# Optimization experiments

Measured on AMD Instinct MI355X. Metric: run time of the kernel, lower is better.

## Reference

```python
import jax, jax.numpy as jnp
import numpy as np
from jax import lax

D_MODEL = 256
VOCAB = 512
D_INNER = 512          # expand=2
D_STATE = 64
D_CONV = 4
HEADDIM = 32
NHEADS = D_INNER // HEADDIM  # 16
NGROUPS = 1
CHUNK = 64
D_IN_PROJ = 2 * D_INNER + 2 * NGROUPS * D_STATE + NHEADS  # 1168
CONV_DIM = D_INNER + 2 * NGROUPS * D_STATE               # 640


def setup_inputs() -> dict:
    key = jax.random.key(0)
    ks = jax.random.split(key, 8)
    B, L = 8, 4096
    input_ids = jax.random.randint(ks[0], (B, L), 0, VOCAB)
    rn = lambda k, shp, sc: (jax.random.normal(k, shp) * sc).astype(jnp.float32)
    embed_w = rn(ks[1], (VOCAB, D_MODEL), 0.02).at[0].set(0.0)  # padding_idx=0
    in_proj_w = rn(ks[2], (D_IN_PROJ, D_MODEL), D_MODEL ** -0.5)
    conv_w = rn(ks[3], (CONV_DIM, D_CONV), 0.2)
    conv_b = jnp.zeros((CONV_DIM,), jnp.float32)
    A_log = jnp.log(jax.random.uniform(ks[4], (NHEADS,), minval=1.0, maxval=16.0)).astype(jnp.float32)
    D_skip = jnp.ones((NHEADS,), jnp.float32)
    dt0 = jax.random.uniform(ks[5], (NHEADS,), minval=1e-3, maxval=0.1)
    dt_bias = jnp.log(jnp.expm1(dt0)).astype(jnp.float32)  # inverse softplus
    gate_norm_w = jnp.ones((D_INNER,), jnp.float32)
    out_proj_w = rn(ks[6], (D_MODEL, D_INNER), D_INNER ** -0.5)
    norm_w = jnp.ones((D_MODEL,), jnp.float32)
    return dict(input_ids=input_ids, embed_w=embed_w, in_proj_w=in_proj_w,
                conv_w=conv_w, conv_b=conv_b, A_log=A_log, D_skip=D_skip,
                dt_bias=dt_bias, gate_norm_w=gate_norm_w, out_proj_w=out_proj_w,
                norm_w=norm_w)


def _rmsnorm(x, w, eps):
    return x * lax.rsqrt(jnp.mean(x * x, axis=-1, keepdims=True) + eps) * w


def _segsum(a):
    # a: (..., T) -> (..., T, T); out[q,s] = sum_{s+1..q} a, -inf above diag
    T = a.shape[-1]
    c = jnp.cumsum(a, axis=-1)
    seg = c[..., :, None] - c[..., None, :]
    mask = jnp.tril(jnp.ones((T, T), bool))
    return jnp.where(mask, seg, -jnp.inf)


def _ssd(X, A, Bm, Cm):
    # X:(b,l,h,p) already *dt ; A:(b,l,h)=dt*A_head ; Bm,Cm:(b,l,n)
    b, l, h, p = X.shape
    n = Bm.shape[-1]
    c, q = l // CHUNK, CHUNK
    X = X.reshape(b, c, q, h, p)
    A = A.reshape(b, c, q, h).transpose(0, 3, 1, 2)        # (b,h,c,q)
    Bm = Bm.reshape(b, c, q, n)
    Cm = Cm.reshape(b, c, q, n)
    A_cs = jnp.cumsum(A, axis=-1)                           # (b,h,c,q)
    Lmat = jnp.exp(_segsum(A))                              # (b,h,c,q,q)
    # intra-chunk (diagonal block) output
    Y_diag = jnp.einsum('bcqn,bckn,bhcqk,bckhp->bcqhp', Cm, Bm, Lmat, X)
    # states carried to end of each chunk
    decay_states = jnp.exp(A_cs[..., -1:] - A_cs)           # (b,h,c,q)
    states = jnp.einsum('bckn,bhck,bckhp->bchpn', Bm, decay_states, X)
    chunk_decay = jnp.exp(A_cs[..., -1])                    # (b,h,c)
    def step(hprev, inp):
        dec, st = inp
        return dec[..., None, None] * hprev + st, hprev
    _, prev = lax.scan(step, jnp.zeros((b, h, p, n), X.dtype),
                       (chunk_decay.transpose(2, 0, 1), states.transpose(1, 0, 2, 3, 4)))
    prev = prev.transpose(1, 0, 2, 3, 4)                    # (b,c,h,p,n)
    Y_off = jnp.einsum('bcqn,bchpn,bhcq->bcqhp', Cm, prev, jnp.exp(A_cs))
    return (Y_diag + Y_off).reshape(b, l, h, p)


def _mamba2(u, in_proj_w, conv_w, conv_b, A_log, D_skip, dt_bias, gate_norm_w, out_proj_w):
    B, L, _ = u.shape
    zxbcdt = u @ in_proj_w.T                                # (B,L,1168)
    z = zxbcdt[..., :D_INNER]
    xBC = zxbcdt[..., D_INNER:D_INNER + CONV_DIM]
    dt = zxbcdt[..., D_INNER + CONV_DIM:]                   # (B,L,H)
    # causal depthwise conv + silu
    xBC = lax.conv_general_dilated(xBC.transpose(0, 2, 1), conv_w[:, None, :],
                                   (1,), [(D_CONV - 1, 0)],
                                   dimension_numbers=('NCH', 'OIH', 'NCH'),
                                   feature_group_count=CONV_DIM)
    xBC = jax.nn.silu(xBC + conv_b[None, :, None]).transpose(0, 2, 1)
    x = xBC[..., :D_INNER].reshape(B, L, NHEADS, HEADDIM)
    Bm = xBC[..., D_INNER:D_INNER + D_STATE]
    Cm = xBC[..., D_INNER + D_STATE:]
    dt = jax.nn.softplus(dt + dt_bias)                      # (B,L,H)
    A = -jnp.exp(A_log)                                     # (H,)
    y = _ssd(x * dt[..., None], dt * A, Bm, Cm)
    y = y + D_skip[None, None, :, None] * x
    y = y.reshape(B, L, D_INNER)
    y = _rmsnorm(y * jax.nn.silu(z), gate_norm_w, 1e-5)     # RMSNormGated
    return y @ out_proj_w.T


def reference(input_ids, embed_w, in_proj_w, conv_w, conv_b, A_log, D_skip,
              dt_bias, gate_norm_w, out_proj_w, norm_w):
    x = embed_w[input_ids]                                  # (B,L,D)
    u = _rmsnorm(x, norm_w, 1e-6)
    x = x + _mamba2(u, in_proj_w, conv_w, conv_b, A_log, D_skip,
                    dt_bias, gate_norm_w, out_proj_w)
    logits = x @ embed_w.T                                  # tied lm_head
    return logits
```

## Files before the change

### kernel.cpp

```cpp
#include <hip/hip_runtime.h>
#include <cstdint>
#include <cstddef>

#define TOK    32768
#define BATCH  8
#define SEQ    4096
#define DMODEL 256
#define DINNER 512
#define DSTATE 64
#define NH     16
#define HD     32
#define DPROJ  1168
#define NPAD   1280
#define CONVD  640
#define VOCAB  512
#define HGRP   4
#define TS     132

typedef __attribute__((ext_vector_type(8))) short bf16x8;
typedef __attribute__((ext_vector_type(4))) float f32x4;

__device__ __forceinline__ unsigned short f2bf(float f) {
    unsigned u = __float_as_uint(f);
    u += 0x7fffu + ((u >> 16) & 1u);
    return (unsigned short)(u >> 16);
}
__device__ __forceinline__ float bf2f(short s) {
    return __uint_as_float(((unsigned)(unsigned short)s) << 16);
}
__device__ __forceinline__ unsigned cvtpk(float lo, float hi) {
    unsigned r;
    asm("v_cvt_pk_bf16_f32 %0, %1, %2" : "=v"(r) : "v"(lo), "v"(hi));
    return r;
}
__device__ __forceinline__ float fsilu(float s) {
    return s * __builtin_amdgcn_rcpf(1.f + __expf(-s));
}
__device__ __forceinline__ float sp(float v) {
    return v > 20.f ? v : __logf(1.f + __expf(v));
}

__device__ __forceinline__ void gload16(const short* src, short* dst) {
    __builtin_amdgcn_global_load_lds((const __attribute__((address_space(1))) void*)src,
                                     (__attribute__((address_space(3))) void*)dst, 16, 0, 0);
}

#define U16_OFF   0
#define Z16_OFF   (U16_OFF  + (size_t)TOK*128)
#define XBC_OFF   (Z16_OFF  + (size_t)TOK*256)
#define DTS_OFF   (XBC_OFF  + (size_t)TOK*320)
#define ACS_OFF   (DTS_OFF  + (size_t)TOK*16)
#define CDEC_OFF  (ACS_OFF  + (size_t)BATCH*NH*64*64)
#define WP_OFF    (CDEC_OFF + (size_t)BATCH*NH*64)
#define WO_OFF    (WP_OFF   + 163840)
#define WE_OFF    (WO_OFF   + 65536)
#define UNION_OFF (WE_OFF   + 65536)
#define UNION_FL  ((size_t)BATCH*64*NH*2048)
#define XF_SUB    ((size_t)TOK*256)
#define WS_FLOATS (UNION_OFF + UNION_FL)

__global__ void k_diag(float* out, float wsmb) {
    if (blockIdx.x == 0 && threadIdx.x == 0) out[0] = wsmb;
}

__global__ void k_cvt(const float* __restrict__ s, short* __restrict__ d, int nsrc, int ntot) {
    int i = blockIdx.x * 256 + threadIdx.x;
    if (i < ntot) d[i] = (i < nsrc) ? (short)f2bf(s[i]) : (short)0;
}

__global__ void k_embed(const int* __restrict__ ids, const float* __restrict__ embed,
                        const float* __restrict__ norm_w, short* __restrict__ u16) {
    int t = blockIdx.x;
    int lane = threadIdx.x;
    int id = ids[t];
    float4 v = ((const float4*)(embed + (size_t)id * DMODEL))[lane];
    float ss = v.x*v.x + v.y*v.y + v.z*v.z + v.w*v.w;
    #pragma unroll
    for (int o = 32; o > 0; o >>= 1) ss += __shfl_down(ss, o);
    ss = __shfl(ss, 0);
    float r = rsqrtf(ss * (1.0f / DMODEL) + 1e-6f);
    float4 w = ((const float4*)norm_w)[lane];
    unsigned p0 = cvtpk(v.x * r * w.x, v.y * r * w.y);
    unsigned p1 = cvtpk(v.z * r * w.z, v.w * r * w.w);
    ((uint2*)(u16 + (size_t)t * DMODEL))[lane] = make_uint2(p0, p1);
}

template<int MODE>
__global__ __launch_bounds__(512) void k_gemm_mfma(
    const short* __restrict__ A, const short* __restrict__ B, int K,
    float* __restrict__ outF, short* __restrict__ z16, short* __restrict__ xbc,
    float* __restrict__ dts, const float* __restrict__ dt_bias,
    const int* __restrict__ ids, const float* __restrict__ embed,
    const float* __restrict__ cw, const float* __restrict__ cb) {
    __shared__ __align__(16) short SM[32768];
    int tid = threadIdx.x;
    int m0 = blockIdx.y << 7;
    int n0 = blockIdx.x << 7;
    int wave = tid >> 6, lane = tid & 63;
    int wm = wave >> 1, wn = wave & 1;
    int lr = lane & 15, lg = lane >> 4;
    const f32x4 zer = {0.f, 0.f, 0.f, 0.f};
    f32x4 acc[2][4];
    #pragma unroll
    for (int i = 0; i < 2; i++)
        #pragma unroll
        for (int j = 0; j < 4; j++) acc[i][j] = zer;

    const bool isXBC = (MODE == 0) && (n0 >= 512) && (n0 < 1152);
    const bool atStart = (m0 & (SEQ - 1)) == 0;
    const bool haloLane = isXBC && (wm == 0) && !atStart && (lr < 3);
    f32x4 hacc[4];
    #pragma unroll
    for (int j = 0; j < 4; j++) hacc[j] = zer;
    const bf16x8 hz = {0, 0, 0, 0, 0, 0, 0, 0};
    bf16x8 hc0 = hz, hc1 = hz, hn0 = hz, hn1 = hz;

    const int nK = K >> 6;
    const int slo = lane >> 3;
    const int skb = ((lane & 7) ^ slo) << 3;

    {
        #pragma unroll
        for (int j = 0; j < 2; j++) {
            int row = wave * 16 + j * 8 + slo;
            gload16(A + (size_t)(m0 + row) * K + skb, SM + (wave * 2 + j) * 512);
            gload16(B + (size_t)(n0 + row) * K + skb, SM + 16384 + (wave * 2 + j) * 512);
        }
        if (haloLane) {
            hc0 = *(const bf16x8*)(A + (size_t)(m0 - 3 + lr) * K + lg * 8);
            hc1 = *(const bf16x8*)(A + (size_t)(m0 - 3 + lr) * K + 32 + lg * 8);
        }
    }
    __syncthreads();

    for (int kt = 0; kt < nK; ++kt) {
        if (kt + 1 < nK) {
            int k0 = (kt + 1) << 6;
            int nb = ((kt + 1) & 1) * 8192;
            #pragma unroll
            for (int j = 0; j < 2; j++) {
                int row = wave * 16 + j * 8 + slo;
                gload16(A + (size_t)(m0 + row) * K + k0 + skb, SM + nb + (wave * 2 + j) * 512);
                gload16(B + (size_t)(n0 + row) * K + k0 + skb, SM + 16384 + nb + (wave * 2 + j) * 512);
            }
            if (haloLane) {
                hn0 = *(const bf16x8*)(A + (size_t)(m0 - 3 + lr) * K + k0 + lg * 8);
                hn1 = *(const bf16x8*)(A + (size_t)(m0 - 3 + lr) * K + k0 + 32 + lg * 8);
            }
        }
        const short* CA = SM + (kt & 1) * 8192;
        const short* CB = SM + 16384 + (kt & 1) * 8192;
        #pragma unroll
        for (int kk = 0; kk < 2; kk++) {
            int sw = (((kk << 2) + lg) ^ (lr & 7)) << 3;
            bf16x8 af[2], bfr[4];
            #pragma unroll
            for (int mi = 0; mi < 2; mi++)
                af[mi] = *(const bf16x8*)&CA[(wm * 32 + mi * 16 + lr) * 64 + sw];
            #pragma unroll
            for (int ni = 0; ni < 4; ni++)
                bfr[ni] = *(const bf16x8*)&CB[(wn * 64 + ni * 16 + lr) * 64 + sw];
            #pragma unroll
            for (int mi = 0; mi < 2; mi++)
                #pragma unroll
                for (int ni = 0; ni < 4; ni++)
                    acc[mi][ni] = __builtin_amdgcn_mfma_f32_16x16x32_bf16(af[mi], bfr[ni], acc[mi][ni], 0, 0, 0);
            if (isXBC && wm == 0) {
                bf16x8 h = (kk == 0) ? hc0 : hc1;
                #pragma unroll
                for (int ni = 0; ni < 4; ni++)
                    hacc[ni] = __builtin_amdgcn_mfma_f32_16x16x32_bf16(h, bfr[ni], hacc[ni], 0, 0, 0);
            }
        }
        __syncthreads();
        hc0 = hn0; hc1 = hn1;
    }

    if (isXBC) {
        short* Tile = SM;
        #pragma unroll
        for (int mi = 0; mi < 2; mi++)
            #pragma unroll
            for (int ni = 0; ni < 4; ni++)
                #pragma unroll
                for (int r = 0; r < 4; r++) {
                    int row = wm * 32 + mi * 16 + lg * 4 + r;
                    int col = wn * 64 + ni * 16 + lr;
                    float v = acc[mi][ni][r];
                    float vo = __shfl_xor(v, 1);
                    if (!(lr & 1))
                        *(unsigned*)&Tile[(3 + row) * TS + col] = cvtpk(v, vo);
                }
        if (wm == 0 && lg == 0) {
            #pragma unroll
            for (int ni = 0; ni < 4; ni++)
                #pragma unroll
                for (int r = 0; r < 3; r++)
                    Tile[r * TS + wn * 64 + ni * 16 + lr] = (short)f2bf(hacc[ni][r]);
        }
        __syncthreads();
        int cp = tid & 63, rg = tid >> 6;
        int colb = cp * 2;
        int ch = (n0 - 512) + colb;
        float c0w0 = cw[ch * 4], c0w1 = cw[ch * 4 + 1], c0w2 = cw[ch * 4 + 2], c0w3 = cw[ch * 4 + 3];
        float c1w0 = cw[ch * 4 + 4], c1w1 = cw[ch * 4 + 5], c1w2 = cw[ch * 4 + 6], c1w3 = cw[ch * 4 + 7];
        float b0v = cb[ch], b1v = cb[ch + 1];
        int rbase = rg * 16;
        unsigned w0 = *(const unsigned*)&Tile[(rbase + 0) * TS + colb];
        unsigned w1 = *(const unsigned*)&Tile[(rbase + 1) * TS + colb];
        unsigned w2 = *(const unsigned*)&Tile[(rbase + 2) * TS + colb];
        for (int i = 0; i < 16; i++) {
            unsigned w3 = *(const unsigned*)&Tile[(rbase + i + 3) * TS + colb];
            float s0 = b0v, s1 = b1v;
            s0 = fmaf(bf2f((short)(w0 & 0xffffu)), c0w0, s0); s1 = fmaf(bf2f((short)(w0 >> 16)), c1w0, s1);
            s0 = fmaf(bf2f((short)(w1 & 0xffffu)), c0w1, s0); s1 = fmaf(bf2f((short)(w1 >> 16)), c1w1, s1);
            s0 = fmaf(bf2f((short)(w2 & 0xffffu)), c0w2, s0); s1 = fmaf(bf2f((short)(w2 >> 16)), c1w2, s1);
            s0 = fmaf(bf2f((short)(w3 & 0xffffu)), c0w3, s0); s1 = fmaf(bf2f((short)(w3 >> 16)), c1w3, s1);
            s0 = fsilu(s0);
            s1 = fsilu(s1);
            *(unsigned*)&xbc[(size_t)(m0 + rbase + i) * CONVD + ch] = cvtpk(s0, s1);
            w0 = w1; w1 = w2; w2 = w3;
        }
        return;
    }

    #pragma unroll
    for (int mi = 0; mi < 2; mi++) {
        #pragma unroll
        for (int r = 0; r < 4; r++) {
            int row = m0 + wm * 32 + mi * 16 + lg * 4 + r;
            int id = 0;
            if (MODE == 1) id = ids[row];
            #pragma unroll
            for (int ni = 0; ni < 4; ni++) {
                int col = n0 + wn * 64 + ni * 16 + lr;
                float v = acc[mi][ni][r];
                if (MODE == 0) {
                    if (n0 < 512) {
                        float vo = __shfl_xor(v, 1);
                        if (!(lr & 1))
                            *(unsigned*)&z16[(size_t)row * DINNER + col] = cvtpk(v, vo);
                    } else if (wn == 0 && ni == 0) {
                        dts[(size_t)row * NH + lr] = sp(v + dt_bias[lr]);
                    }
                } else if (MODE == 1) {
                    float vo = __shfl_xor(v, 1);
                    if (!(lr & 1)) {
                        float2 res = *(const float2*)&embed[(size_t)id * DMODEL + col];
                        *(unsigned*)&z16[(size_t)row * DMODEL + col] = cvtpk(v + res.x, vo + res.y);
                    }
                } else {
                    outF[(size_t)row * VOCAB + col] = v;
                }
            }
        }
    }
}

__global__ __launch_bounds__(256) void k_states(const short* __restrict__ xbc, const float* __restrict__ dts,
                                                const float* __restrict__ A_log,
                                                short* __restrict__ st16,
                                                float* __restrict__ acs_g, float* __restrict__ cdec) {
    __shared__ short BsB[64 * 72];
    __shared__ short BT[64 * 72];
    __shared__ short XdS[32 * 72];
    __shared__ float dkS[HGRP][64];
    int tid = threadIdx.x;
    int bid = blockIdx.x;
    int hg = bid & 3;
    int bc = bid >> 2;
    int b = bc >> 6, c = bc & 63;
    int h0 = hg * HGRP;
    size_t tbase = (size_t)b * SEQ + (size_t)c * 64;
    int wave = tid >> 6, lane = tid & 63;
    int lr = lane & 15, lg = lane >> 4;

    for (int i = tid; i < 64 * 64; i += 256) {
        int q = i >> 6, n = i & 63;
        BsB[q * 72 + n] = xbc[(tbase + q) * CONVD + DINNER + n];
    }
    {
        int h = h0 + wave;
        float Ah = -__expf(A_log[h]);
        float v = dts[(tbase + lane) * NH + h] * Ah;
        #pragma unroll
        for (int off = 1; off < 64; off <<= 1) {
            float o = __shfl_up(v, off);
            if (lane >= off) v += o;
        }
        acs_g[(((size_t)(b * NH + h)) * 64 + c) * 64 + lane] = v;
        float alast = __shfl(v, 63);
        dkS[wave][lane] = __expf(alast - v);
        if (lane == 0) cdec[(b * NH + h) * 64 + c] = __expf(alast);
    }
    __syncthreads();
    for (int i = tid; i < 64 * 64; i += 256) {
        int k = i >> 6, n = i & 63;
        BT[n * 72 + k] = BsB[k * 72 + n];
    }
    __syncthreads();

    for (int hh = 0; hh < HGRP; hh++) {
        int h = h0 + hh;
        for (int i = tid; i < 2048; i += 256) {
            int p = i & 31, k = i >> 5;
            float xv = bf2f(xbc[(tbase + k) * CONVD + h * HD + p]);
            XdS[p * 72 + k] = (short)f2bf(xv * dts[(tbase + k) * NH + h] * dkS[hh][k]);
        }
        __syncthreads();
        {
            int ptile = wave & 1;
            bf16x8 a0 = *(const bf16x8*)&XdS[(ptile * 16 + lr) * 72 + lg * 8];
            bf16x8 a1 = *(const bf16x8*)&XdS[(ptile * 16 + lr) * 72 + 32 + lg * 8];
            size_t base = ((size_t)bc * NH + h) * 2048;
            #pragma unroll
            for (int j = 0; j < 2; j++) {
                int nt = (wave >> 1) * 2 + j;
                bf16x8 b0 = *(const bf16x8*)&BT[(nt * 16 + lr) * 72 + lg * 8];
                bf16x8 b1 = *(const bf16x8*)&BT[(nt * 16 + lr) * 72 + 32 + lg * 8];
                f32x4 z = {0.f, 0.f, 0.f, 0.f};
                z = __builtin_amdgcn_mfma_f32_16x16x32_bf16(a0, b0, z, 0, 0, 0);
                z = __builtin_amdgcn_mfma_f32_16x16x32_bf16(a1, b1, z, 0, 0, 0);
                #pragma unroll
                for (int r = 0; r < 4; r++) {
                    int p = ptile * 16 + lg * 4 + r;
                    float v = z[r];
                    float vo = __shfl_xor(v, 1);
                    if (!(lr & 1))
                        *(unsigned*)&st16[base + p * 64 + nt * 16 + lr] = cvtpk(v, vo);
                }
            }
        }
        __syncthreads();
    }
}

__global__ __launch_bounds__(256) void k_scan(unsigned* __restrict__ st32, const float* __restrict__ cdec) {
    int bid = blockIdx.x;
    int bh = bid >> 2, seg = bid & 3;
    int b = bh >> 4, h = bh & 15;
    int off = seg * 256 + threadIdx.x;
    float p0 = 0.f, p1 = 0.f;
    for (int c = 0; c < 64; c++) {
        float dec = cdec[bh * 64 + c];
        size_t idx = ((((size_t)b * 64 + c) * NH) + h) * 1024 + off;
        unsigned v = st32[idx];
        float s0 = bf2f((short)(v & 0xffffu));
        float s1 = bf2f((short)(v >> 16));
        st32[idx] = cvtpk(p0, p1);
        p0 = fmaf(dec, p0, s0);
        p1 = fmaf(dec, p1, s1);
    }
}

__global__ __launch_bounds__(256) void k_y(const short* __restrict__ xbc, const float* __restrict__ dts,
                                           const short* __restrict__ st16, const float* __restrict__ acs_g,
                                           const float* __restrict__ D_skip, float* __restrict__ Y) {
    __shared__ short CsB[64 * 72];
    __shared__ short BsB[64 * 72];
    __shared__ short Wsh[64 * 72];
    __shared__ short XtS[32 * 72];
    __shared__ short Pt[32 * 72];
    __shared__ float acsS[HGRP][64];
    int tid = threadIdx.x;
    int bid = blockIdx.x;
    int hg = bid & 3;
    int bc = bid >> 2;
    int b = bc >> 6, c = bc & 63;
    int h0 = hg * HGRP;
    size_t tbase = (size_t)b * SEQ + (size_t)c * 64;
    int wave = tid >> 6, lane = tid & 63;
    int lr = lane & 15, lg = lane >> 4;

    for (int i = tid; i < 64 * 64; i += 256) {
        int q = i >> 6, n = i & 63;
        const short* rowp = xbc + (tbase + q) * CONVD + DINNER;
        BsB[q * 72 + n] = rowp[n];
        CsB[q * 72 + n] = rowp[DSTATE + n];
    }
    acsS[wave][lane] = acs_g[(((size_t)(b * NH + h0 + wave)) * 64 + c) * 64 + lane];
    __syncthreads();

    f32x4 macc[4];
    {
        bf16x8 aw0 = *(const bf16x8*)&CsB[(wave * 16 + lr) * 72 + lg * 8];
        bf16x8 aw1 = *(const bf16x8*)&CsB[(wave * 16 + lr) * 72 + 32 + lg * 8];
        #pragma unroll
        for (int ct = 0; ct < 4; ct++) {
            bf16x8 b0 = *(const bf16x8*)&BsB[(ct * 16 + lr) * 72 + lg * 8];
            bf16x8 b1 = *(const bf16x8*)&BsB[(ct * 16 + lr) * 72 + 32 + lg * 8];
            f32x4 z = {0.f, 0.f, 0.f, 0.f};
            z = __builtin_amdgcn_mfma_f32_16x16x32_bf16(aw0, b0, z, 0, 0, 0);
            z = __builtin_amdgcn_mfma_f32_16x16x32_bf16(aw1, b1, z, 0, 0, 0);
            macc[ct] = z;
        }
    }

    for (int hh = 0; hh < HGRP; hh++) {
        int h = h0 + hh;
        #pragma unroll
        for (int ct = 0; ct < 4; ct++) {
            int k = ct * 16 + lr;
            #pragma unroll
            for (int r = 0; r < 4; r++) {
                int q = wave * 16 + lg * 4 + r;
                float wv = 0.f;
                if (k <= q) wv = macc[ct][r] * __expf(acsS[hh][q] - acsS[hh][k]);
                float wo = __shfl_xor(wv, 1);
                if (!(lr & 1))
                    *(unsigned*)&Wsh[q * 72 + k] = cvtpk(wv, wo);
            }
        }
        for (int i = tid; i < 2048; i += 256) {
            int p = i & 31, k = i >> 5;
            float xv = bf2f(xbc[(tbase + k) * CONVD + h * HD + p]);
            XtS[p * 72 + k] = (short)f2bf(xv * dts[(tbase + k) * NH + h]);
        }
        size_t sbase = ((size_t)bc * NH + h) * 2048;
        for (int i = tid; i < 2048; i += 256)
            Pt[(i >> 6) * 72 + (i & 63)] = st16[sbase + i];
        __syncthreads();
        float eq[4];
        #pragma unroll
        for (int r = 0; r < 4; r++) eq[r] = __expf(acsS[hh][wave * 16 + lg * 4 + r]);
        float dsk = D_skip[h];
        bf16x8 wa0 = *(const bf16x8*)&Wsh[(wave * 16 + lr) * 72 + lg * 8];
        bf16x8 wa1 = *(const bf16x8*)&Wsh[(wave * 16 + lr) * 72 + 32 + lg * 8];
        bf16x8 ca0 = *(const bf16x8*)&CsB[(wave * 16 + lr) * 72 + lg * 8];
        bf16x8 ca1 = *(const bf16x8*)&CsB[(wave * 16 + lr) * 72 + 32 + lg * 8];
        #pragma unroll
        for (int pt = 0; pt < 2; pt++) {
            bf16x8 xb0 = *(const bf16x8*)&XtS[(pt * 16 + lr) * 72 + lg * 8];
            bf16x8 xb1 = *(const bf16x8*)&XtS[(pt * 16 + lr) * 72 + 32 + lg * 8];
            f32x4 zd = {0.f, 0.f, 0.f, 0.f};
            zd = __builtin_amdgcn_mfma_f32_16x16x32_bf16(wa0, xb0, zd, 0, 0, 0);
            zd = __builtin_amdgcn_mfma_f32_16x16x32_bf16(wa1, xb1, zd, 0, 0, 0);
            bf16x8 pb0 = *(const bf16x8*)&Pt[(pt * 16 + lr) * 72 + lg * 8];
            bf16x8 pb1 = *(const bf16x8*)&Pt[(pt * 16 + lr) * 72 + 32 + lg * 8];
            f32x4 zo = {0.f, 0.f, 0.f, 0.f};
            zo = __builtin_amdgcn_mfma_f32_16x16x32_bf16(ca0, pb0, zo, 0, 0, 0);
            zo = __builtin_amdgcn_mfma_f32_16x16x32_bf16(ca1, pb1, zo, 0, 0, 0);
            #pragma unroll
            for (int r = 0; r < 4; r++) {
                int q = wave * 16 + lg * 4 + r;
                int p = pt * 16 + lr;
                float xv = bf2f(xbc[(tbase + q) * CONVD + h * HD + p]);
                Y[((tbase + q) * NH + h) * HD + p] = zd[r] + eq[r] * zo[r] + dsk * xv;
            }
        }
        __syncthreads();
    }
}

__global__ void k_gate(const float* __restrict__ Y, const short* __restrict__ z16,
                       const float* __restrict__ gw, short* __restrict__ Yb) {
    int t = blockIdx.x;
    int lane = threadIdx.x;
    const float* yr = Y + (size_t)t * DINNER + lane * 8;
    union { int4 v; short s[8]; } zu;
    zu.v = *(const int4*)(z16 + (size_t)t * DINNER + lane * 8);
    float4 y0 = *(const float4*)yr;
    float4 y1 = *(const float4*)(yr + 4);
    float yv[8] = {y0.x, y0.y, y0.z, y0.w, y1.x, y1.y, y1.z, y1.w};
    float g[8];
    float ss = 0.f;
    #pragma unroll
    for (int i = 0; i < 8; i++) {
        float zf = bf2f(zu.s[i]);
        g[i] = yv[i] * fsilu(zf);
        ss += g[i] * g[i];
    }
    #pragma unroll
    for (int o = 32; o > 0; o >>= 1) ss += __shfl_down(ss, o);
    ss = __shfl(ss, 0);
    float rr = rsqrtf(ss * (1.0f / DINNER) + 1e-5f);
    const float* wr = gw + lane * 8;
    float4 w0 = *(const float4*)wr;
    float4 w1 = *(const float4*)(wr + 4);
    float wv[8] = {w0.x, w0.y, w0.z, w0.w, w1.x, w1.y, w1.z, w1.w};
    union { uint4 v; unsigned u[4]; } ou;
    #pragma unroll
    for (int i = 0; i < 4; i++)
        ou.u[i] = cvtpk(g[2*i] * rr * wv[2*i], g[2*i+1] * rr * wv[2*i+1]);
    *(uint4*)(Yb + (size_t)t * DINNER + lane * 8) = ou.v;
}

extern "C" void kernel_launch(void* const* d_in, const int* in_sizes, int n_in,
                              void* d_out, int out_size, void* d_ws, size_t ws_size,
                              hipStream_t stream) {
    const int*   ids        = (const int*)d_in[0];
    const float* embed_w    = (const float*)d_in[1];
    const float* in_proj_w  = (const float*)d_in[2];
    const float* conv_w     = (const float*)d_in[3];
    const float* conv_b     = (const float*)d_in[4];
    const float* A_log      = (const float*)d_in[5];
    const float* D_skip     = (const float*)d_in[6];
    const float* dt_bias    = (const float*)d_in[7];
    const float* gate_w     = (const float*)d_in[8];
    const float* out_proj_w = (const float*)d_in[9];
    const float* norm_w     = (const float*)d_in[10];
    float* out = (float*)d_out;

    if (ws_size < WS_FLOATS * sizeof(float)) {
        k_diag<<<1, 64, 0, stream>>>(out, (float)(ws_size >> 20));
        return;
    }

    float* ws   = (float*)d_ws;
    short* u16  = (short*)(ws + U16_OFF);
    short* z16  = (short*)(ws + Z16_OFF);
    short* xbc  = (short*)(ws + XBC_OFF);
    float* dts  = ws + DTS_OFF;
    float* acs  = ws + ACS_OFF;
    float* cdec = ws + CDEC_OFF;
    short* Wp   = (short*)(ws + WP_OFF);
    short* Wo   = (short*)(ws + WO_OFF);
    short* We   = (short*)(ws + WE_OFF);
    short* st16 = (short*)(ws + UNION_OFF);
    short* Yb   = (short*)(ws + UNION_OFF);
    short* xf16 = (short*)(ws + UNION_OFF + XF_SUB);
    float* Y    = out;

    k_cvt<<<(NPAD * DMODEL + 255) / 256, 256, 0, stream>>>(in_proj_w, Wp, DPROJ * DMODEL, NPAD * DMODEL);
    k_cvt<<<(DMODEL * DINNER + 255) / 256, 256, 0, stream>>>(out_proj_w, Wo, DMODEL * DINNER, DMODEL * DINNER);
    k_cvt<<<(VOCAB * DMODEL + 255) / 256, 256, 0, stream>>>(embed_w, We, VOCAB * DMODEL, VOCAB * DMODEL);
    k_embed<<<TOK, 64, 0, stream>>>(ids, embed_w, norm_w, u16);
    k_gemm_mfma<0><<<dim3(NPAD / 128, TOK / 128), 512, 0, stream>>>(
        u16, Wp, DMODEL, nullptr, z16, xbc, dts, dt_bias, nullptr, nullptr, conv_w, conv_b);
    k_states<<<BATCH * 64 * 4, 256, 0, stream>>>(xbc, dts, A_log, st16, acs, cdec);
    k_scan<<<BATCH * NH * 4, 256, 0, stream>>>((unsigned*)st16, cdec);
    k_y<<<BATCH * 64 * 4, 256, 0, stream>>>(xbc, dts, st16, acs, D_skip, Y);
    k_gate<<<TOK, 64, 0, stream>>>(Y, z16, gate_w, Yb);
    k_gemm_mfma<1><<<dim3(DMODEL / 128, TOK / 128), 512, 0, stream>>>(
        Yb, Wo, DINNER, nullptr, xf16, nullptr, nullptr, nullptr, ids, embed_w, nullptr, nullptr);
    k_gemm_mfma<2><<<dim3(VOCAB / 128, TOK / 128), 512, 0, stream>>>(
        xf16, We, DMODEL, out, nullptr, nullptr, nullptr, nullptr, nullptr, nullptr, nullptr, nullptr);
}
```

Baseline: 255.5 us.

## Store SSD output as bf16 and process heads in pairs to halve barriers

k_y now writes its per-head output as packed bf16 into workspace instead of fp32 into the output buffer, and k_gate reads bf16, which halves the intermediate Y traffic. Both k_states and k_y now stage two heads per iteration with double LDS buffers, halving the number of __syncthreads rounds and giving more independent MFMA work between barriers. k_y also hoists the C-operand fragments out of the head loop. The cost is extra LDS per block, which may lower occupancy, and an added bf16 rounding of Y before the gated RMSNorm.

```diff
diff --git a/kernel.cpp b/kernel.cpp
--- a/kernel.cpp
+++ b/kernel.cpp
@@ -56,6 +56,7 @@
 #define WE_OFF    (WO_OFF   + 65536)
 #define UNION_OFF (WE_OFF   + 65536)
 #define UNION_FL  ((size_t)BATCH*64*NH*2048)
+#define Y16_SUB   ((size_t)TOK*256)
 #define XF_SUB    ((size_t)TOK*256)
 #define WS_FLOATS (UNION_OFF + UNION_FL)
 
@@ -263,7 +264,8 @@
                                                 float* __restrict__ acs_g, float* __restrict__ cdec) {
     __shared__ short BsB[64 * 72];
     __shared__ short BT[64 * 72];
-    __shared__ short XdS[32 * 72];
+    __shared__ short Xd0[32 * 72];
+    __shared__ short Xd1[32 * 72];
     __shared__ float dkS[HGRP][64];
     int tid = threadIdx.x;
     int bid = blockIdx.x;
@@ -300,37 +302,44 @@
     }
     __syncthreads();
 
-    for (int hh = 0; hh < HGRP; hh++) {
-        int h = h0 + hh;
+    auto do_head = [&](int h, const short* Xd) {
+        int ptile = wave & 1;
+        bf16x8 a0 = *(const bf16x8*)&Xd[(ptile * 16 + lr) * 72 + lg * 8];
+        bf16x8 a1 = *(const bf16x8*)&Xd[(ptile * 16 + lr) * 72 + 32 + lg * 8];
+        size_t base = ((size_t)bc * NH + h) * 2048;
+        #pragma unroll
+        for (int j = 0; j < 2; j++) {
+            int nt = (wave >> 1) * 2 + j;
+            bf16x8 b0 = *(const bf16x8*)&BT[(nt * 16 + lr) * 72 + lg * 8];
+            bf16x8 b1 = *(const bf16x8*)&BT[(nt * 16 + lr) * 72 + 32 + lg * 8];
+            f32x4 z = {0.f, 0.f, 0.f, 0.f};
+            z = __builtin_amdgcn_mfma_f32_16x16x32_bf16(a0, b0, z, 0, 0, 0);
+            z = __builtin_amdgcn_mfma_f32_16x16x32_bf16(a1, b1, z, 0, 0, 0);
+            #pragma unroll
+            for (int r = 0; r < 4; r++) {
+                int p = ptile * 16 + lg * 4 + r;
+                float v = z[r];
+                float vo = __shfl_xor(v, 1);
+                if (!(lr & 1))
+                    *(unsigned*)&st16[base + p * 64 + nt * 16 + lr] = cvtpk(v, vo);
+            }
+        }
+    };
+
+    #pragma unroll
+    for (int pr = 0; pr < HGRP / 2; pr++) {
+        int hhA = pr * 2, hhB = hhA + 1;
+        int hA = h0 + hhA, hB = h0 + hhB;
         for (int i = tid; i < 2048; i += 256) {
             int p = i & 31, k = i >> 5;
-            float xv = bf2f(xbc[(tbase + k) * CONVD + h * HD + p]);
-            XdS[p * 72 + k] = (short)f2bf(xv * dts[(tbase + k) * NH + h] * dkS[hh][k]);
+            float dtA = dts[(tbase + k) * NH + hA];
+            float dtB = dts[(tbase + k) * NH + hB];
+            Xd0[p * 72 + k] = (short)f2bf(bf2f(xbc[(tbase + k) * CONVD + hA * HD + p]) * dtA * dkS[hhA][k]);
+            Xd1[p * 72 + k] = (short)f2bf(bf2f(xbc[(tbase + k) * CONVD + hB * HD + p]) * dtB * dkS[hhB][k]);
         }
         __syncthreads();
-        {
-            int ptile = wave & 1;
-            bf16x8 a0 = *(const bf16x8*)&XdS[(ptile * 16 + lr) * 72 + lg * 8];
-            bf16x8 a1 = *(const bf16x8*)&XdS[(ptile * 16 + lr) * 72 + 32 + lg * 8];
-            size_t base = ((size_t)bc * NH + h) * 2048;
-            #pragma unroll
-            for (int j = 0; j < 2; j++) {
-                int nt = (wave >> 1) * 2 + j;
-                bf16x8 b0 = *(const bf16x8*)&BT[(nt * 16 + lr) * 72 + lg * 8];
-                bf16x8 b1 = *(const bf16x8*)&BT[(nt * 16 + lr) * 72 + 32 + lg * 8];
-                f32x4 z = {0.f, 0.f, 0.f, 0.f};
-                z = __builtin_amdgcn_mfma_f32_16x16x32_bf16(a0, b0, z, 0, 0, 0);
-                z = __builtin_amdgcn_mfma_f32_16x16x32_bf16(a1, b1, z, 0, 0, 0);
-                #pragma unroll
-                for (int r = 0; r < 4; r++) {
-                    int p = ptile * 16 + lg * 4 + r;
-                    float v = z[r];
-                    float vo = __shfl_xor(v, 1);
-                    if (!(lr & 1))
-                        *(unsigned*)&st16[base + p * 64 + nt * 16 + lr] = cvtpk(v, vo);
-                }
-            }
-        }
+        do_head(hA, Xd0);
+        do_head(hB, Xd1);
         __syncthreads();
     }
 }
@@ -355,12 +364,12 @@
 
 __global__ __launch_bounds__(256) void k_y(const short* __restrict__ xbc, const float* __restrict__ dts,
                                            const short* __restrict__ st16, const float* __restrict__ acs_g,
-                                           const float* __restrict__ D_skip, float* __restrict__ Y) {
+                                           const float* __restrict__ D_skip, short* __restrict__ Y16) {
     __shared__ short CsB[64 * 72];
-    __shared__ short BsB[64 * 72];
-    __shared__ short Wsh[64 * 72];
-    __shared__ short XtS[32 * 72];
-    __shared__ short Pt[32 * 72];
+    __shared__ short W0[64 * 72];
+    __shared__ short W1[64 * 72];
+    __shared__ short Xt0[32 * 72], Xt1[32 * 72];
+    __shared__ short Pt0[32 * 72], Pt1[32 * 72];
     __shared__ float acsS[HGRP][64];
     int tid = threadIdx.x;
     int bid = blockIdx.x;
@@ -375,29 +384,29 @@
     for (int i = tid; i < 64 * 64; i += 256) {
         int q = i >> 6, n = i & 63;
         const short* rowp = xbc + (tbase + q) * CONVD + DINNER;
-        BsB[q * 72 + n] = rowp[n];
+        W0[q * 72 + n]  = rowp[n];
         CsB[q * 72 + n] = rowp[DSTATE + n];
     }
     acsS[wave][lane] = acs_g[(((size_t)(b * NH + h0 + wave)) * 64 + c) * 64 + lane];
     __syncthreads();
 
     f32x4 macc[4];
+    bf16x8 ca0 = *(const bf16x8*)&CsB[(wave * 16 + lr) * 72 + lg * 8];
+    bf16x8 ca1 = *(const bf16x8*)&CsB[(wave * 16 + lr) * 72 + 32 + lg * 8];
     {
-        bf16x8 aw0 = *(const bf16x8*)&CsB[(wave * 16 + lr) * 72 + lg * 8];
-        bf16x8 aw1 = *(const bf16x8*)&CsB[(wave * 16 + lr) * 72 + 32 + lg * 8];
         #pragma unroll
         for (int ct = 0; ct < 4; ct++) {
-            bf16x8 b0 = *(const bf16x8*)&BsB[(ct * 16 + lr) * 72 + lg * 8];
-            bf16x8 b1 = *(const bf16x8*)&BsB[(ct * 16 + lr) * 72 + 32 + lg * 8];
+            bf16x8 b0 = *(const bf16x8*)&W0[(ct * 16 + lr) * 72 + lg * 8];
+            bf16x8 b1 = *(const bf16x8*)&W0[(ct * 16 + lr) * 72 + 32 + lg * 8];
             f32x4 z = {0.f, 0.f, 0.f, 0.f};
-            z = __builtin_amdgcn_mfma_f32_16x16x32_bf16(aw0, b0, z, 0, 0, 0);
-            z = __builtin_amdgcn_mfma_f32_16x16x32_bf16(aw1, b1, z, 0, 0, 0);
+            z = __builtin_amdgcn_mfma_f32_16x16x32_bf16(ca0, b0, z, 0, 0, 0);
+            z = __builtin_amdgcn_mfma_f32_16x16x32_bf16(ca1, b1, z, 0, 0, 0);
             macc[ct] = z;
         }
     }
-
-    for (int hh = 0; hh < HGRP; hh++) {
-        int h = h0 + hh;
+    __syncthreads();
+
+    auto build_w = [&](int hh, short* Wb) {
         #pragma unroll
         for (int ct = 0; ct < 4; ct++) {
             int k = ct * 16 + lr;
@@ -408,30 +417,21 @@
                 if (k <= q) wv = macc[ct][r] * __expf(acsS[hh][q] - acsS[hh][k]);
                 float wo = __shfl_xor(wv, 1);
                 if (!(lr & 1))
-                    *(unsigned*)&Wsh[q * 72 + k] = cvtpk(wv, wo);
-            }
-        }
-        for (int i = tid; i < 2048; i += 256) {
-            int p = i & 31, k = i >> 5;
-            float xv = bf2f(xbc[(tbase + k) * CONVD + h * HD + p]);
-            XtS[p * 72 + k] = (short)f2bf(xv * dts[(tbase + k) * NH + h]);
-        }
-        size_t sbase = ((size_t)bc * NH + h) * 2048;
-        for (int i = tid; i < 2048; i += 256)
-            Pt[(i >> 6) * 72 + (i & 63)] = st16[sbase + i];
-        __syncthreads();
+                    *(unsigned*)&Wb[q * 72 + k] = cvtpk(wv, wo);
+            }
+        }
+    };
+    auto do_head = [&](int h, int hh, const short* Wb, const short* Xt, const short* Pt) {
         float eq[4];
         #pragma unroll
         for (int r = 0; r < 4; r++) eq[r] = __expf(acsS[hh][wave * 16 + lg * 4 + r]);
         float dsk = D_skip[h];
-        bf16x8 wa0 = *(const bf16x8*)&Wsh[(wave * 16 + lr) * 72 + lg * 8];
-        bf16x8 wa1 = *(const bf16x8*)&Wsh[(wave * 16 + lr) * 72 + 32 + lg * 8];
-        bf16x8 ca0 = *(const bf16x8*)&CsB[(wave * 16 + lr) * 72 + lg * 8];
-        bf16x8 ca1 = *(const bf16x8*)&CsB[(wave * 16 + lr) * 72 + 32 + lg * 8];
+        bf16x8 wa0 = *(const bf16x8*)&Wb[(wave * 16 + lr) * 72 + lg * 8];
+        bf16x8 wa1 = *(const bf16x8*)&Wb[(wave * 16 + lr) * 72 + 32 + lg * 8];
         #pragma unroll
         for (int pt = 0; pt < 2; pt++) {
-            bf16x8 xb0 = *(const bf16x8*)&XtS[(pt * 16 + lr) * 72 + lg * 8];
-            bf16x8 xb1 = *(const bf16x8*)&XtS[(pt * 16 + lr) * 72 + 32 + lg * 8];
+            bf16x8 xb0 = *(const bf16x8*)&Xt[(pt * 16 + lr) * 72 + lg * 8];
+            bf16x8 xb1 = *(const bf16x8*)&Xt[(pt * 16 + lr) * 72 + 32 + lg * 8];
             f32x4 zd = {0.f, 0.f, 0.f, 0.f};
             zd = __builtin_amdgcn_mfma_f32_16x16x32_bf16(wa0, xb0, zd, 0, 0, 0);
             zd = __builtin_amdgcn_mfma_f32_16x16x32_bf16(wa1, xb1, zd, 0, 0, 0);
@@ -445,29 +445,52 @@
                 int q = wave * 16 + lg * 4 + r;
                 int p = pt * 16 + lr;
                 float xv = bf2f(xbc[(tbase + q) * CONVD + h * HD + p]);
-                Y[((tbase + q) * NH + h) * HD + p] = zd[r] + eq[r] * zo[r] + dsk * xv;
-            }
+                float v = zd[r] + eq[r] * zo[r] + dsk * xv;
+                float vo = __shfl_xor(v, 1);
+                if (!(lr & 1))
+                    *(unsigned*)&Y16[((tbase + q) * NH + h) * HD + p] = cvtpk(v, vo);
+            }
+        }
+    };
+
+    #pragma unroll
+    for (int pr = 0; pr < HGRP / 2; pr++) {
+        int hhA = pr * 2, hhB = hhA + 1;
+        int hA = h0 + hhA, hB = h0 + hhB;
+        build_w(hhA, W0);
+        build_w(hhB, W1);
+        for (int i = tid; i < 2048; i += 256) {
+            int p = i & 31, k = i >> 5;
+            float dtA = dts[(tbase + k) * NH + hA];
+            float dtB = dts[(tbase + k) * NH + hB];
+            Xt0[p * 72 + k] = (short)f2bf(bf2f(xbc[(tbase + k) * CONVD + hA * HD + p]) * dtA);
+            Xt1[p * 72 + k] = (short)f2bf(bf2f(xbc[(tbase + k) * CONVD + hB * HD + p]) * dtB);
+        }
+        size_t sbA = ((size_t)bc * NH + hA) * 2048;
+        for (int i = tid; i < 2048; i += 256) {
+            Pt0[(i >> 6) * 72 + (i & 63)] = st16[sbA + i];
+            Pt1[(i >> 6) * 72 + (i & 63)] = st16[sbA + 2048 + i];
         }
         __syncthreads();
-    }
-}
-
-__global__ void k_gate(const float* __restrict__ Y, const short* __restrict__ z16,
+        do_head(hA, hhA, W0, Xt0, Pt0);
+        do_head(hB, hhB, W1, Xt1, Pt1);
+        __syncthreads();
+    }
+}
+
+__global__ void k_gate(const short* __restrict__ Y16, const short* __restrict__ z16,
                        const float* __restrict__ gw, short* __restrict__ Yb) {
     int t = blockIdx.x;
     int lane = threadIdx.x;
-    const float* yr = Y + (size_t)t * DINNER + lane * 8;
-    union { int4 v; short s[8]; } zu;
+    union { int4 v; short s[8]; } zu, yu;
     zu.v = *(const int4*)(z16 + (size_t)t * DINNER + lane * 8);
-    float4 y0 = *(const float4*)yr;
-    float4 y1 = *(const float4*)(yr + 4);
-    float yv[8] = {y0.x, y0.y, y0.z, y0.w, y1.x, y1.y, y1.z, y1.w};
+    yu.v = *(const int4*)(Y16 + (size_t)t * DINNER + lane * 8);
     float g[8];
     float ss = 0.f;
     #pragma unroll
     for (int i = 0; i < 8; i++) {
         float zf = bf2f(zu.s[i]);
-        g[i] = yv[i] * fsilu(zf);
+        g[i] = bf2f(yu.s[i]) * fsilu(zf);
         ss += g[i] * g[i];
     }
     #pragma unroll
@@ -517,9 +540,11 @@
     short* Wo   = (short*)(ws + WO_OFF);
     short* We   = (short*)(ws + WE_OFF);
     short* st16 = (short*)(ws + UNION_OFF);
+    short* Y16  = (short*)(ws + UNION_OFF + Y16_SUB);
     short* Yb   = (short*)(ws + UNION_OFF);
     short* xf16 = (short*)(ws + UNION_OFF + XF_SUB);
     float* Y    = out;
+    (void)Y;
 
     k_cvt<<<(NPAD * DMODEL + 255) / 256, 256, 0, stream>>>(in_proj_w, Wp, DPROJ * DMODEL, NPAD * DMODEL);
     k_cvt<<<(DMODEL * DINNER + 255) / 256, 256, 0, stream>>>(out_proj_w, Wo, DMODEL * DINNER, DMODEL * DINNER);
@@ -529,8 +554,8 @@
         u16, Wp, DMODEL, nullptr, z16, xbc, dts, dt_bias, nullptr, nullptr, conv_w, conv_b);
     k_states<<<BATCH * 64 * 4, 256, 0, stream>>>(xbc, dts, A_log, st16, acs, cdec);
     k_scan<<<BATCH * NH * 4, 256, 0, stream>>>((unsigned*)st16, cdec);
-    k_y<<<BATCH * 64 * 4, 256, 0, stream>>>(xbc, dts, st16, acs, D_skip, Y);
-    k_gate<<<TOK, 64, 0, stream>>>(Y, z16, gate_w, Yb);
+    k_y<<<BATCH * 64 * 4, 256, 0, stream>>>(xbc, dts, st16, acs, D_skip, Y16);
+    k_gate<<<TOK, 64, 0, stream>>>(Y16, z16, gate_w, Yb);
     k_gemm_mfma<1><<<dim3(DMODEL / 128, TOK / 128), 512, 0, stream>>>(
         Yb, Wo, DINNER, nullptr, xf16, nullptr, nullptr, nullptr, ids, embed_w, nullptr, nullptr);
     k_gemm_mfma<2><<<dim3(VOCAB / 128, TOK / 128), 512, 0, stream>>>(
```

After: 253.4 us. About the same (-0.8%).
